# Performance work log

Hardware: AMD Instinct MI355X
Metric: run time of the kernel (lower is better)

## Reference

```python
import jax, jax.numpy as jnp
import numpy as np

B, L, E, H, W = 2, 8192, 1024, 16, 128
HD = E // H  # 64


def setup_inputs() -> dict:
    key = jax.random.key(0)
    ks = jax.random.split(key, 9)
    s = 1.0 / np.sqrt(E)
    inp = {"x": jax.random.normal(ks[0], (B, L, E), jnp.float32)}
    for i, n in enumerate(["Wq", "Wk", "Wv", "Wo"]):
        inp[n] = jax.random.uniform(ks[1 + i], (E, E), jnp.float32, -s, s)
    for i, n in enumerate(["bq", "bk", "bv", "bo"]):
        inp[n] = jax.random.uniform(ks[5 + i], (E,), jnp.float32, -s, s)
    return inp


def _skew_prob(p, w):
    # (..., w, 2w+1) -> (..., w, 3w) with row i right-shifted by i:
    # out[..., i, i+j] = p[..., i, j]  (zeros elsewhere)
    lead = p.shape[:-2]
    M, Lc = p.shape[-2], p.shape[-1]
    p = jnp.pad(p, [(0, 0)] * len(lead) + [(0, 0), (0, M + 1)])
    p = p.reshape(*lead, M * (Lc + M + 1))[..., :-M].reshape(*lead, M, M + Lc)
    return p[..., :-1]


def _sliding_attend(q, k, v, w):
    # q,k,v: (b,h,l,d); banded attention, window w on each side (2w+1 diagonals)
    b, h, l, d = q.shape
    c = l // w
    qc = q.reshape(b, h, c, w, d)
    # per-chunk key/value windows of 3w tokens (w halo each side, zero padded)
    idx = jnp.arange(c)[:, None] * w + jnp.arange(3 * w)[None, :]  # (c, 3w)
    kw = jnp.pad(k, ((0, 0), (0, 0), (w, w), (0, 0)))[:, :, idx]  # (b,h,c,3w,d)
    s = jnp.einsum('bhcqd,bhckd->bhcqk', qc, kw)  # (b,h,c,w,3w)
    # extract band: band[i, j] = s[i, i+j], j in [0, 2w] (offset d = j - w)
    gidx = (jnp.arange(w)[:, None] + jnp.arange(2 * w + 1)[None, :])[None, None, None]
    band = jnp.take_along_axis(s, gidx, axis=-1).reshape(b, h, l, 2 * w + 1)
    # mask out-of-range positions (matches the module's edge -inf loop)
    pos = jnp.arange(l)[:, None] + (jnp.arange(2 * w + 1) - w)[None, :]
    band = jnp.where((pos >= 0) & (pos < l), band, -jnp.inf)
    prob = jax.nn.softmax(band / np.sqrt(d), axis=-1)  # scale by sqrt(head_dim)
    vw = jnp.pad(v, ((0, 0), (0, 0), (w, w), (0, 0)))[:, :, idx]  # (b,h,c,3w,d)
    p3 = _skew_prob(prob.reshape(b, h, c, w, 2 * w + 1), w)  # (b,h,c,w,3w)
    ctx = jnp.einsum('bhcqk,bhckd->bhcqd', p3, vw)
    return ctx.reshape(b, h, l, d)


def reference(x, Wq, Wk, Wv, Wo, bq, bk, bv, bo):
    q = (x @ Wq.T + bq).reshape(B, L, H, HD).transpose(0, 2, 1, 3)
    k = (x @ Wk.T + bk).reshape(B, L, H, HD).transpose(0, 2, 1, 3)
    v = (x @ Wv.T + bv).reshape(B, L, H, HD).transpose(0, 2, 1, 3)
    ctx = _sliding_attend(q, k, v, W)
    ctx = ctx.transpose(0, 2, 1, 3).reshape(B, L, E)
    return ctx @ Wo.T + bo
```

## Files before the change

### kernel.cpp

```cpp
#include <hip/hip_runtime.h>
#include <math.h>

#define B_SZ  2
#define L_SEQ 8192
#define EMB   1024
#define NH    16
#define HDIM  64
#define WIN   128
#define MROWS (B_SZ*L_SEQ)

typedef __attribute__((ext_vector_type(8))) _Float16 f16x8;
typedef __attribute__((ext_vector_type(4))) _Float16 f16x4;
typedef __attribute__((ext_vector_type(4))) float f32x4;

__device__ __forceinline__ void gload16(const void* g, void* l) {
    __builtin_amdgcn_global_load_lds(
        (const __attribute__((address_space(1))) unsigned int*)g,
        (__attribute__((address_space(3))) unsigned int*)l, 16, 0, 0);
}

__global__ __launch_bounds__(256)
void round_all(const float* __restrict__ x,
               const float* __restrict__ wq, const float* __restrict__ wk,
               const float* __restrict__ wv, const float* __restrict__ wo,
               _Float16* __restrict__ xf, _Float16* __restrict__ q16,
               _Float16* __restrict__ k16, _Float16* __restrict__ v16,
               _Float16* __restrict__ o16)
{
    const size_t NX = (size_t)MROWS * EMB, NW = (size_t)EMB * EMB;
    size_t gid = ((size_t)blockIdx.x * 256 + threadIdx.x) * 4;
    const float* src; _Float16* dst; size_t off;
    if (gid < NX)               { src = x;  dst = xf;  off = gid; }
    else if (gid < NX + NW)     { src = wq; dst = q16; off = gid - NX; }
    else if (gid < NX + 2*NW)   { src = wk; dst = k16; off = gid - NX - 2*NW + NW; }
    else if (gid < NX + 3*NW)   { src = wv; dst = v16; off = gid - NX - 2*NW; }
    else                        { src = wo; dst = o16; off = gid - NX - 3*NW; }
    float4 v = *(const float4*)(src + off);
    f16x4 o;
    o[0] = (_Float16)v.x; o[1] = (_Float16)v.y;
    o[2] = (_Float16)v.z; o[3] = (_Float16)v.w;
    *(f16x4*)(dst + off) = o;
}


#define QKV_LOOP_PROLOGUE(Aptr, Bptr)                                          \
    const int t = threadIdx.x;                                                 \
    const int wave = t >> 6, lane = t & 63;                                    \
    const int wr = wave >> 2, wc = wave & 3;                                   \
    const int frow = lane & 15, quad = lane >> 4;                              \
    const int srow = t >> 2;                                                   \
    const int schunk = (t & 3) ^ ((t >> 3) & 3);                               \
    size_t gA[2], gB[2];                                                       \
    _Pragma("unroll")                                                          \
    for (int s = 0; s < 2; ++s) {                                              \
        int r = s * 128 + srow;                                                \
        gA[s] = (size_t)(bm + r) * 1024 + schunk * 8;                          \
        gB[s] = (size_t)(bn + r) * 1024 + schunk * 8;                          \
    }                                                                          \
    const int ldst = t * 16;                                                   \
    const int sw = (quad ^ ((frow >> 1) & 3)) * 16;                            \
    int aoff[8], boff[4];                                                      \
    _Pragma("unroll")                                                          \
    for (int i = 0; i < 8; ++i) aoff[i] = (wr * 128 + i * 16 + frow) * 64 + sw;\
    _Pragma("unroll")                                                          \
    for (int j = 0; j < 4; ++j)                                                \
        boff[j] = 32768 + (wc * 64 + j * 16 + frow) * 64 + sw;                 \
    f32x4 acc[8][4] = {};                                                      \
    _Pragma("unroll")                                                          \
    for (int pt = 0; pt < 2; ++pt)                                             \
        _Pragma("unroll")                                                      \
        for (int s = 0; s < 2; ++s) {                                          \
            gload16(Aptr + gA[s] + pt * 32, smem + pt * 16384 + s * 8192 + ldst);          \
            gload16(Bptr + gB[s] + pt * 32, smem + 32768 + pt * 16384 + s * 8192 + ldst);  \
        }                                                                      \
    for (int kt = 0; kt < 32; ++kt) {                                          \
        const int cur = kt & 1;                                                \
        if (kt < 31) asm volatile("s_waitcnt vmcnt(4)");                       \
        else         asm volatile("s_waitcnt vmcnt(0)");                       \
        __builtin_amdgcn_s_barrier();                                          \
        asm volatile("" ::: "memory");                                         \
        const char* Ab = (const char*)smem + cur * 16384;                      \
        f16x8 af[4], bf[4];                                                    \
        _Pragma("unroll")                                                      \
        for (int j = 0; j < 4; ++j) bf[j] = *(const f16x8*)(Ab + boff[j] * 2 - boff[j] + boff[j]); \
        _Pragma("unroll")                                                      \
        for (int j = 0; j < 4; ++j) bf[j] = *(const f16x8*)(Ab + boff[j]);     \
        _Pragma("unroll")                                                      \
        for (int i = 0; i < 4; ++i) af[i] = *(const f16x8*)(Ab + aoff[i] * 1); \
        __builtin_amdgcn_s_setprio(1);                                         \
        _Pragma("unroll")                                                      \
        for (int i = 0; i < 4; ++i)                                            \
            _Pragma("unroll")                                                  \
            for (int j = 0; j < 4; ++j)                                        \
                acc[i][j] = __builtin_amdgcn_mfma_f32_16x16x32_f16(af[i], bf[j], acc[i][j], 0, 0, 0); \
        __builtin_amdgcn_s_setprio(0);                                         \
        _Pragma("unroll")                                                      \
        for (int i = 0; i < 4; ++i) af[i] = *(const f16x8*)(Ab + aoff[i + 4]); \
        __builtin_amdgcn_s_setprio(1);                                         \
        _Pragma("unroll")                                                      \
        for (int i = 0; i < 4; ++i)                                            \
            _Pragma("unroll")                                                  \
            for (int j = 0; j < 4; ++j)                                        \
                acc[i + 4][j] = __builtin_amdgcn_mfma_f32_16x16x32_f16(af[i], bf[j], acc[i + 4][j], 0, 0, 0); \
        __builtin_amdgcn_s_setprio(0);                                         \
        asm volatile("" ::: "memory");                                         \
        __builtin_amdgcn_s_barrier();                                          \
        asm volatile("" ::: "memory");                                         \
        if (kt + 2 < 32) {                                                     \
            const int ko = (kt + 2) * 32;                                      \
            _Pragma("unroll")                                                  \
            for (int s = 0; s < 2; ++s) {                                      \
                gload16(Aptr + gA[s] + ko, smem + cur * 16384 + s * 8192 + ldst);          \
                gload16(Bptr + gB[s] + ko, smem + 32768 + cur * 16384 + s * 8192 + ldst);  \
            }                                                                  \
        }                                                                      \
    }


__global__ __launch_bounds__(512, 2)
void gemm_qkv(const _Float16* __restrict__ X,
              const _Float16* __restrict__ Wq, const _Float16* __restrict__ Wk,
              const _Float16* __restrict__ Wv,
              const float* __restrict__ bq, const float* __restrict__ bk,
              const float* __restrict__ bv,
              _Float16* __restrict__ qf, _Float16* __restrict__ kf,
              _Float16* __restrict__ vtf)
{
    __shared__ __attribute__((aligned(16))) char smem[65536];

    const int id = blockIdx.x;
    const int row = (id / 96) * 8 + (id & 7);
    const int colq = (id >> 3) % 12;
    const int wsel = colq >> 2;
    const int bm = row * 256, bn = (colq & 3) * 256;
    const _Float16* Bw = wsel == 0 ? Wq : wsel == 1 ? Wk : Wv;
    const float* bias = wsel == 0 ? bq : wsel == 1 ? bk : bv;
    const float scale = wsel == 0 ? 0.125f : 1.0f;

    QKV_LOOP_PROLOGUE(X, Bw)

    char* Cw = smem + wave * 8192;
    const int bb = bm >> 13;
    const int l0 = (bm & (L_SEQ - 1)) + wr * 128;
    const int h = (bn >> 6) + wc;
    if (wsel < 2) {
        _Float16* dst = wsel == 0 ? qf : kf;
        const size_t hb = ((size_t)(bb * NH + h)) * L_SEQ * HDIM;
        #pragma unroll
        for (int ih = 0; ih < 2; ++ih) {
            asm volatile("" ::: "memory");
            #pragma unroll
            for (int i = 0; i < 4; ++i)
                #pragma unroll
                for (int j = 0; j < 4; ++j) {
                    const int lc = j * 16 + frow;
                    const float bvv = bias[bn + wc * 64 + lc];
                    #pragma unroll
                    for (int r = 0; r < 4; ++r) {
                        const int lr = i * 16 + quad * 4 + r;
                        const int bo = lr * 128 + ((lc * 2) ^ ((lr & 7) << 4));
                        *(_Float16*)(Cw + bo) = (_Float16)((acc[ih * 4 + i][j][r] + bvv) * scale);
                    }
                }
            asm volatile("" ::: "memory");
            #pragma unroll
            for (int p = 0; p < 8; ++p) {
                const int idx = p * 64 + lane;
                const int lr = idx >> 3, seg = idx & 7;
                const int bo = lr * 128 + ((seg * 16) ^ ((lr & 7) << 4));
                uint4 v = *(const uint4*)(Cw + bo);
                *(uint4*)&dst[hb + (size_t)(l0 + ih * 64 + lr) * HDIM + seg * 8] = v;
            }
        }
    } else {
        const size_t hb = ((size_t)(bb * NH + h)) * HDIM * L_SEQ;
        #pragma unroll
        for (int ih = 0; ih < 2; ++ih) {
            asm volatile("" ::: "memory");
            #pragma unroll
            for (int i = 0; i < 4; ++i)
                #pragma unroll
                for (int j = 0; j < 4; ++j) {
                    const int lc = j * 16 + frow;
                    const float bvv = bias[bn + wc * 64 + lc];
                    #pragma unroll
                    for (int r = 0; r < 4; ++r) {
                        const int lr = i * 16 + quad * 4 + r;
                        const int bo = lc * 128 + ((lr * 2) ^ ((lc & 7) << 4));
                        *(_Float16*)(Cw + bo) = (_Float16)(acc[ih * 4 + i][j][r] + bvv);
                    }
                }
            asm volatile("" ::: "memory");
            #pragma unroll
            for (int p = 0; p < 8; ++p) {
                const int idx = p * 64 + lane;
                const int dc = idx >> 3, sl = idx & 7;
                const int bo = dc * 128 + ((sl * 16) ^ ((dc & 7) << 4));
                uint4 v = *(const uint4*)(Cw + bo);
                *(uint4*)&vtf[hb + (size_t)dc * L_SEQ + (l0 + ih * 64 + sl * 8)] = v;
            }
        }
    }
}

__global__ __launch_bounds__(512, 2)
void gemm_out(const _Float16* __restrict__ A, const _Float16* __restrict__ Bwm,
              const float* __restrict__ bias, float* __restrict__ C)
{
    constexpr int N = EMB;
    __shared__ __attribute__((aligned(16))) char smem[65536];

    const int id = blockIdx.x;
    const int row = (id / 32) * 8 + (id & 7);
    const int bm = row * 256, bn = ((id >> 3) & 3) * 256;

    QKV_LOOP_PROLOGUE(A, Bwm)

    #pragma unroll
    for (int i = 0; i < 8; ++i) {
        int m0 = bm + wr * 128 + i * 16 + quad * 4;
        #pragma unroll
        for (int j = 0; j < 4; ++j) {
            int n = bn + wc * 64 + j * 16 + frow;
            float bvv = bias[n];
            #pragma unroll
            for (int r = 0; r < 4; ++r)
                C[(size_t)(m0 + r) * N + n] = acc[i][j][r] + bvv;
        }
    }
}

__global__ __launch_bounds__(256)
void attn_mfma(const _Float16* __restrict__ qf, const _Float16* __restrict__ kf,
               const _Float16* __restrict__ vtf, _Float16* __restrict__ cf)
{
    __shared__ _Float16 Kf[4096], Vf[4096];
    __shared__ _Float16 Ps[4][16 * 72];

    const int t = threadIdx.x;
    const int wave = t >> 6, lane = t & 63;
    const int col = lane & 15, quad = lane >> 4;
    const int bh = blockIdx.y;
    const int q0 = blockIdx.x * 128;

    f16x8 qfr[2][2];
    #pragma unroll
    for (int g = 0; g < 2; g++) {
        size_t qidx = ((size_t)bh * L_SEQ + q0 + g * 64 + wave * 16 + col) * HDIM + quad * 8;
        qfr[g][0] = *(const f16x8*)(qf + qidx);
        qfr[g][1] = *(const f16x8*)(qf + qidx + 32);
    }

    f32x4 o[2][4] = {};
    float mrun[2][4], lrun[2][4];
    #pragma unroll
    for (int g = 0; g < 2; g++)
        #pragma unroll
        for (int r = 0; r < 4; r++) { mrun[g][r] = -3e38f; lrun[g][r] = 0.0f; }

    const int srow = t >> 3, sc = t & 7;
    _Float16* Pw = Ps[wave];

    for (int kt = 0; kt < 6; kt++) {
        const int p0 = q0 - WIN + kt * 64;
        if (p0 < 0 || p0 >= L_SEQ) continue;
        #pragma unroll
        for (int sw2 = 0; sw2 < 2; sw2++) {
            int row = sw2 * 32 + srow;
            int gq = sc ^ (row & 7);
            size_t kgi = ((size_t)bh * L_SEQ + p0 + row) * HDIM + gq * 8;
            size_t vgi = ((size_t)bh * HDIM + row) * L_SEQ + p0 + gq * 8;
            int lb = sw2 * 4096 + wave * 1024;
            gload16(kf + kgi, (char*)Kf + lb);
            gload16(vtf + vgi, (char*)Vf + lb);
        }
        __syncthreads();

        #pragma unroll
        for (int g = 0; g < 2; g++) {
            f32x4 s[4] = {};
            #pragma unroll
            for (int ks = 0; ks < 2; ks++)
                #pragma unroll
                for (int n = 0; n < 4; n++) {
                    int off = (n * 16 + col) * 128 + (((ks * 4 + quad) ^ (col & 7)) * 16);
                    f16x8 kfr = *(const f16x8*)((const char*)Kf + off);
                    s[n] = __builtin_amdgcn_mfma_f32_16x16x32_f16(qfr[g][ks], kfr, s[n], 0, 0, 0);
                }
            const int rowb = q0 + g * 64 + wave * 16 + quad * 4;
            #pragma unroll
            for (int n = 0; n < 4; n++)
                #pragma unroll
                for (int r = 0; r < 4; r++) {
                    int dlt = (p0 + n * 16 + col) - (rowb + r);
                    if (dlt < -WIN || dlt > WIN) s[n][r] = -3e38f;
                }
            float mx[4];
            #pragma unroll
            for (int r = 0; r < 4; r++)
                mx[r] = fmaxf(fmaxf(s[0][r], s[1][r]), fmaxf(s[2][r], s[3][r]));
            #pragma unroll
            for (int x = 1; x < 16; x <<= 1)
                #pragma unroll
                for (int r = 0; r < 4; r++)
                    mx[r] = fmaxf(mx[r], __shfl_xor(mx[r], x, 64));
            float alpha[4];
            #pragma unroll
            for (int r = 0; r < 4; r++) {
                float mn = fmaxf(mrun[g][r], mx[r]);
                alpha[r] = __expf(mrun[g][r] - mn);
                mrun[g][r] = mn;
            }
            float sm[4] = {0.f, 0.f, 0.f, 0.f};
            #pragma unroll
            for (int n = 0; n < 4; n++)
                #pragma unroll
                for (int r = 0; r < 4; r++) {
                    float pv = __expf(s[n][r] - mrun[g][r]);
                    sm[r] += pv;
                    Pw[(quad * 4 + r) * 72 + n * 16 + col] = (_Float16)pv;
                }
            #pragma unroll
            for (int x = 1; x < 16; x <<= 1)
                #pragma unroll
                for (int r = 0; r < 4; r++)
                    sm[r] += __shfl_xor(sm[r], x, 64);
            #pragma unroll
            for (int r = 0; r < 4; r++)
                lrun[g][r] = lrun[g][r] * alpha[r] + sm[r];
            #pragma unroll
            for (int n = 0; n < 4; n++)
                #pragma unroll
                for (int r = 0; r < 4; r++)
                    o[g][n][r] *= alpha[r];
            #pragma unroll
            for (int ks = 0; ks < 2; ks++) {
                f16x8 pfr = *(const f16x8*)&Pw[col * 72 + ks * 32 + quad * 8];
                #pragma unroll
                for (int n = 0; n < 4; n++) {
                    int off = (n * 16 + col) * 128 + (((ks * 4 + quad) ^ (col & 7)) * 16);
                    f16x8 vfr = *(const f16x8*)((const char*)Vf + off);
                    o[g][n] = __builtin_amdgcn_mfma_f32_16x16x32_f16(pfr, vfr, o[g][n], 0, 0, 0);
                }
            }
        }
        __syncthreads();
    }

    const int b = bh >> 4, h = bh & 15;
    #pragma unroll
    for (int g = 0; g < 2; g++)
        #pragma unroll
        for (int r = 0; r < 4; r++) {
            float inv = 1.0f / lrun[g][r];
            int q = q0 + g * 64 + wave * 16 + quad * 4 + r;
            size_t base = ((size_t)b * L_SEQ + q) * EMB + h * HDIM;
            #pragma unroll
            for (int n = 0; n < 4; n++)
                cf[base + n * 16 + col] = (_Float16)(o[g][n][r] * inv);
        }
}

extern "C" void kernel_launch(void* const* d_in, const int* in_sizes, int n_in,
                              void* d_out, int out_size, void* d_ws, size_t ws_size,
                              hipStream_t stream) {
    const float* x  = (const float*)d_in[0];
    const float* Wq = (const float*)d_in[1];
    const float* Wk = (const float*)d_in[2];
    const float* Wv = (const float*)d_in[3];
    const float* Wo = (const float*)d_in[4];
    const float* bq = (const float*)d_in[5];
    const float* bk = (const float*)d_in[6];
    const float* bv = (const float*)d_in[7];
    const float* bo = (const float*)d_in[8];
    float* out = (float*)d_out;

    const size_t per = (size_t)B_SZ * NH * L_SEQ * HDIM;
    _Float16* w16 = (_Float16*)d_ws;
    _Float16* xf   = w16;
    _Float16* qf   = w16 + per;
    _Float16* kf   = w16 + 2 * per;
    _Float16* vtf  = w16 + 3 * per;
    _Float16* cf   = w16 + 4 * per;
    _Float16* wq16 = w16 + 5 * per;
    _Float16* wk16 = wq16 + 1048576;
    _Float16* wv16 = wq16 + 2 * 1048576;
    _Float16* wo16 = wq16 + 3 * 1048576;

    const int nround = (MROWS * EMB + 4 * EMB * EMB) / 1024;
    round_all<<<nround, dim3(256), 0, stream>>>(x, Wq, Wk, Wv, Wo, xf, wq16, wk16, wv16, wo16);

    gemm_qkv<<<768, dim3(512), 0, stream>>>(xf, wq16, wk16, wv16, bq, bk, bv, qf, kf, vtf);

    attn_mfma<<<dim3(L_SEQ / 128, B_SZ * NH), dim3(256), 0, stream>>>(qf, kf, vtf, cf);

    gemm_out<<<256, dim3(512), 0, stream>>>(cf, wo16, bo, out);
}
```

Measured before the change: 381.4 us.

## Double-buffer K/V tiles in attention and restructure GEMM prefetch issue order

The attention kernel now keeps two LDS buffers for K and V. The next 64-key tile is loaded while the current one is computed, instead of a load then __syncthreads per tile. The out-of-range tile skip is replaced by precomputed loop bounds at the sequence edges. The shared GEMM core changes from a depth-2 prefetch issued after the compute barrier to a depth-1 prefetch issued at the top of each iteration, and a redundant duplicate B-fragment load is removed. The GEMM change lowers the prefetch distance, which could expose more load latency.

Result: faster. 368.4 us (-3.4%).

```diff
diff --git a/kernel.cpp b/kernel.cpp
--- a/kernel.cpp
+++ b/kernel.cpp
@@ -43,7 +43,7 @@
 }
 
 
-#define QKV_LOOP_PROLOGUE(Aptr, Bptr)                                          \
+#define GEMM_CORE(Aptr, Bptr)                                                  \
     const int t = threadIdx.x;                                                 \
     const int wave = t >> 6, lane = t & 63;                                    \
     const int wr = wave >> 2, wc = wave & 3;                                   \
@@ -67,26 +67,31 @@
         boff[j] = 32768 + (wc * 64 + j * 16 + frow) * 64 + sw;                 \
     f32x4 acc[8][4] = {};                                                      \
     _Pragma("unroll")                                                          \
-    for (int pt = 0; pt < 2; ++pt)                                             \
-        _Pragma("unroll")                                                      \
-        for (int s = 0; s < 2; ++s) {                                          \
-            gload16(Aptr + gA[s] + pt * 32, smem + pt * 16384 + s * 8192 + ldst);          \
-            gload16(Bptr + gB[s] + pt * 32, smem + 32768 + pt * 16384 + s * 8192 + ldst);  \
-        }                                                                      \
+    for (int s = 0; s < 2; ++s) {                                              \
+        gload16(Aptr + gA[s], smem + s * 8192 + ldst);                         \
+        gload16(Bptr + gB[s], smem + 32768 + s * 8192 + ldst);                 \
+    }                                                                          \
     for (int kt = 0; kt < 32; ++kt) {                                          \
         const int cur = kt & 1;                                                \
-        if (kt < 31) asm volatile("s_waitcnt vmcnt(4)");                       \
-        else         asm volatile("s_waitcnt vmcnt(0)");                       \
+        if (kt < 31) {                                                         \
+            const int ko = (kt + 1) * 32;                                      \
+            _Pragma("unroll")                                                  \
+            for (int s = 0; s < 2; ++s) {                                      \
+                gload16(Aptr + gA[s] + ko, smem + (cur ^ 1) * 16384 + s * 8192 + ldst);          \
+                gload16(Bptr + gB[s] + ko, smem + 32768 + (cur ^ 1) * 16384 + s * 8192 + ldst);  \
+            }                                                                  \
+            asm volatile("s_waitcnt vmcnt(4)" ::: "memory");                   \
+        } else {                                                               \
+            asm volatile("s_waitcnt vmcnt(0)" ::: "memory");                   \
+        }                                                                      \
         __builtin_amdgcn_s_barrier();                                          \
         asm volatile("" ::: "memory");                                         \
         const char* Ab = (const char*)smem + cur * 16384;                      \
         f16x8 af[4], bf[4];                                                    \
         _Pragma("unroll")                                                      \
-        for (int j = 0; j < 4; ++j) bf[j] = *(const f16x8*)(Ab + boff[j] * 2 - boff[j] + boff[j]); \
-        _Pragma("unroll")                                                      \
         for (int j = 0; j < 4; ++j) bf[j] = *(const f16x8*)(Ab + boff[j]);     \
         _Pragma("unroll")                                                      \
-        for (int i = 0; i < 4; ++i) af[i] = *(const f16x8*)(Ab + aoff[i] * 1); \
+        for (int i = 0; i < 4; ++i) af[i] = *(const f16x8*)(Ab + aoff[i]);     \
         __builtin_amdgcn_s_setprio(1);                                         \
         _Pragma("unroll")                                                      \
         for (int i = 0; i < 4; ++i)                                            \
@@ -106,16 +111,7 @@
         asm volatile("" ::: "memory");                                         \
         __builtin_amdgcn_s_barrier();                                          \
         asm volatile("" ::: "memory");                                         \
-        if (kt + 2 < 32) {                                                     \
-            const int ko = (kt + 2) * 32;                                      \
-            _Pragma("unroll")                                                  \
-            for (int s = 0; s < 2; ++s) {                                      \
-                gload16(Aptr + gA[s] + ko, smem + cur * 16384 + s * 8192 + ldst);          \
-                gload16(Bptr + gB[s] + ko, smem + 32768 + cur * 16384 + s * 8192 + ldst);  \
-            }                                                                  \
-        }                                                                      \
-    }
-
+    }
 
 __global__ __launch_bounds__(512, 2)
 void gemm_qkv(const _Float16* __restrict__ X,
@@ -137,7 +133,7 @@
     const float* bias = wsel == 0 ? bq : wsel == 1 ? bk : bv;
     const float scale = wsel == 0 ? 0.125f : 1.0f;
 
-    QKV_LOOP_PROLOGUE(X, Bw)
+    GEMM_CORE(X, Bw)
 
     char* Cw = smem + wave * 8192;
     const int bb = bm >> 13;
@@ -214,7 +210,7 @@
     const int row = (id / 32) * 8 + (id & 7);
     const int bm = row * 256, bn = ((id >> 3) & 3) * 256;
 
-    QKV_LOOP_PROLOGUE(A, Bwm)
+    GEMM_CORE(A, Bwm)
 
     #pragma unroll
     for (int i = 0; i < 8; ++i) {
@@ -234,7 +230,7 @@
 void attn_mfma(const _Float16* __restrict__ qf, const _Float16* __restrict__ kf,
                const _Float16* __restrict__ vtf, _Float16* __restrict__ cf)
 {
-    __shared__ _Float16 Kf[4096], Vf[4096];
+    __shared__ _Float16 Kf[2][4096], Vf[2][4096];
     __shared__ _Float16 Ps[4][16 * 72];
 
     const int t = threadIdx.x;
@@ -261,20 +257,40 @@
     const int srow = t >> 3, sc = t & 7;
     _Float16* Pw = Ps[wave];
 
-    for (int kt = 0; kt < 6; kt++) {
+    const int ktlo = (q0 == 0) ? 2 : 0;
+    const int kthi = (q0 == L_SEQ - 128) ? 4 : 6;
+
+#define STAGE_KV(kt_, bsel_)                                                   \
+    {                                                                          \
+        const int p0s = q0 - WIN + (kt_) * 64;                                 \
+        _Pragma("unroll")                                                      \
+        for (int sw2 = 0; sw2 < 2; sw2++) {                                    \
+            int rowk = sw2 * 32 + srow;                                        \
+            int gq = sc ^ (rowk & 7);                                          \
+            size_t kgi = ((size_t)bh * L_SEQ + p0s + rowk) * HDIM + gq * 8;    \
+            size_t vgi = ((size_t)bh * HDIM + rowk) * L_SEQ + p0s + gq * 8;    \
+            int lb = sw2 * 4096 + wave * 1024;                                 \
+            gload16(kf + kgi, (char*)&Kf[bsel_][0] + lb);                      \
+            gload16(vtf + vgi, (char*)&Vf[bsel_][0] + lb);                     \
+        }                                                                      \
+    }
+
+    STAGE_KV(ktlo, 0)
+
+    for (int kt = ktlo; kt < kthi; kt++) {
         const int p0 = q0 - WIN + kt * 64;
-        if (p0 < 0 || p0 >= L_SEQ) continue;
-        #pragma unroll
-        for (int sw2 = 0; sw2 < 2; sw2++) {
-            int row = sw2 * 32 + srow;
-            int gq = sc ^ (row & 7);
-            size_t kgi = ((size_t)bh * L_SEQ + p0 + row) * HDIM + gq * 8;
-            size_t vgi = ((size_t)bh * HDIM + row) * L_SEQ + p0 + gq * 8;
-            int lb = sw2 * 4096 + wave * 1024;
-            gload16(kf + kgi, (char*)Kf + lb);
-            gload16(vtf + vgi, (char*)Vf + lb);
-        }
-        __syncthreads();
+        const int cb = (kt - ktlo) & 1;
+        if (kt + 1 < kthi) {
+            STAGE_KV(kt + 1, cb ^ 1)
+            asm volatile("s_waitcnt vmcnt(4)" ::: "memory");
+        } else {
+            asm volatile("s_waitcnt vmcnt(0)" ::: "memory");
+        }
+        __builtin_amdgcn_s_barrier();
+        asm volatile("" ::: "memory");
+
+        const char* Kb = (const char*)&Kf[cb][0];
+        const char* Vb = (const char*)&Vf[cb][0];
 
         #pragma unroll
         for (int g = 0; g < 2; g++) {
@@ -284,7 +300,7 @@
                 #pragma unroll
                 for (int n = 0; n < 4; n++) {
                     int off = (n * 16 + col) * 128 + (((ks * 4 + quad) ^ (col & 7)) * 16);
-                    f16x8 kfr = *(const f16x8*)((const char*)Kf + off);
+                    f16x8 kfr = *(const f16x8*)(Kb + off);
                     s[n] = __builtin_amdgcn_mfma_f32_16x16x32_f16(qfr[g][ks], kfr, s[n], 0, 0, 0);
                 }
             const int rowb = q0 + g * 64 + wave * 16 + quad * 4;
@@ -339,12 +355,14 @@
                 #pragma unroll
                 for (int n = 0; n < 4; n++) {
                     int off = (n * 16 + col) * 128 + (((ks * 4 + quad) ^ (col & 7)) * 16);
-                    f16x8 vfr = *(const f16x8*)((const char*)Vf + off);
+                    f16x8 vfr = *(const f16x8*)(Vb + off);
                     o[g][n] = __builtin_amdgcn_mfma_f32_16x16x32_f16(pfr, vfr, o[g][n], 0, 0, 0);
                 }
             }
         }
-        __syncthreads();
+        asm volatile("" ::: "memory");
+        __builtin_amdgcn_s_barrier();
+        asm volatile("" ::: "memory");
     }
 
     const int b = bh >> 4, h = bh & 15;
```
